# Kernel optimization log

Hardware: AMD Instinct MI355X
Metric: run time of the kernel (lower is better)

## Reference

```python
import jax, jax.numpy as jnp
import numpy as np

# --- MLA config (matches init_kwargs) ---
DIM = 2048
H = 16
KV_RANK = 512
Q_RANK = 1536
ROPE = 64          # qk_rope_head_dim (even)
NOPE = 128         # qk_nope_head_dim
VD = 128           # v_head_dim
THETA = 500000.0
EPS = 1e-6
B, T = 1, 2048
QK_HEAD = NOPE + ROPE  # logits use nope + rope dims


def _rmsnorm(x, w):
    # x float32; RMS over last dim, no mean subtraction
    rms = jax.lax.rsqrt(jnp.mean(x * x, axis=-1, keepdims=True) + EPS)
    return (x * rms) * w


def _rope_tables(t):
    inv_freq = 1.0 / (THETA ** (jnp.arange(0, ROPE, 2, dtype=jnp.float32) / ROPE))  # (ROPE/2,)
    pos = jnp.arange(t, dtype=jnp.float32)
    angles = jnp.outer(pos, inv_freq)  # (T, ROPE/2)
    return jnp.cos(angles), jnp.sin(angles)


def _apply_rope(x, cos, sin):
    # x: (B, T, Hx, D) with adjacent-pair rotation; cos/sin: (T, D/2)
    b, t, h, d = x.shape
    xp = x.reshape(b, t, h, d // 2, 2)
    even, odd = xp[..., 0], xp[..., 1]
    c = cos.reshape(1, t, 1, d // 2)
    s = sin.reshape(1, t, 1, d // 2)
    out = jnp.stack((even * c - odd * s, odd * c + even * s), axis=-1)
    return out.reshape(b, t, h, d)


def setup_inputs() -> dict:
    key = jax.random.key(0)
    ks = jax.random.split(key, 7)
    s = 0.02
    x = jax.random.normal(ks[0], (B, T, DIM), dtype=jnp.float32)
    w_q_down = jax.random.normal(ks[1], (Q_RANK, DIM), dtype=jnp.float32) * s
    q_norm_w = jnp.ones((Q_RANK,), dtype=jnp.float32)
    w_q_up = jax.random.normal(ks[2], (H * (NOPE + ROPE), Q_RANK), dtype=jnp.float32) * s
    w_kv_down = jax.random.normal(ks[3], (KV_RANK + ROPE, DIM), dtype=jnp.float32) * s
    kv_norm_w = jnp.ones((KV_RANK,), dtype=jnp.float32)
    w_kv_up = jax.random.normal(ks[4], (H * (NOPE + VD), KV_RANK), dtype=jnp.float32) * s
    w_o = jax.random.normal(ks[5], (DIM, H * VD), dtype=jnp.float32) * s
    return {"x": x, "w_q_down": w_q_down, "q_norm_w": q_norm_w, "w_q_up": w_q_up,
            "w_kv_down": w_kv_down, "kv_norm_w": kv_norm_w, "w_kv_up": w_kv_up, "w_o": w_o}


def reference(x, w_q_down, q_norm_w, w_q_up, w_kv_down, kv_norm_w, w_kv_up, w_o):
    b, t, _ = x.shape
    # Query path: down-proj -> RMSNorm -> up-proj, split nope/rope
    c_q = _rmsnorm(x @ w_q_down.T, q_norm_w)                       # (B,T,Q_RANK)
    q = (c_q @ w_q_up.T).reshape(b, t, H, NOPE + ROPE)
    q_nope, q_rope = q[..., :NOPE], q[..., NOPE:]
    # KV path: down-proj -> split latent c_kv and shared rope key
    kv = x @ w_kv_down.T                                           # (B,T,KV_RANK+ROPE)
    c_kv = kv[..., :KV_RANK]
    k_rope_raw = kv[..., KV_RANK:].reshape(b, t, 1, ROPE)
    # RoPE (adjacent-pair), start_pos=0
    cos, sin = _rope_tables(t)
    q_rope = _apply_rope(q_rope, cos, sin)
    k_rope = _apply_rope(k_rope_raw, cos, sin)                     # (B,T,1,ROPE) shared head
    # Reconstruct k_nope and v from normalized latent
    kv_up = (_rmsnorm(c_kv, kv_norm_w) @ w_kv_up.T).reshape(b, t, H, NOPE + VD)
    k_nope, v = kv_up[..., :NOPE], kv_up[..., NOPE:]
    # Assemble full q/k (rope key broadcast across heads)
    q_full = jnp.concatenate((q_nope, q_rope), axis=-1)            # (B,T,H,QK_HEAD)
    k_full = jnp.concatenate((k_nope, jnp.broadcast_to(k_rope, (b, t, H, ROPE))), axis=-1)
    # Causal attention
    scale = 1.0 / np.sqrt(QK_HEAD)
    scores = jnp.einsum('bqhd,bkhd->bhqk', q_full, k_full) * scale  # (B,H,T,T)
    causal = jnp.tril(jnp.ones((t, t), dtype=bool))
    scores = jnp.where(causal[None, None], scores, -jnp.inf)
    attn = jax.nn.softmax(scores, axis=-1)
    out = jnp.einsum('bhqk,bkhd->bqhd', attn, v).reshape(b, t, H * VD)
    return out @ w_o.T                                             # (B,T,DIM)
```

## Files before the change

kernel.cpp:

```cpp
#include <hip/hip_runtime.h>
#include <hip/hip_bf16.h>

typedef short short8 __attribute__((ext_vector_type(8)));
typedef float f32x4 __attribute__((ext_vector_type(4)));

#define DIM 2048
#define NH 16
#define KV_RANK 512
#define Q_RANK 1536
#define ROPE_D 64
#define NOPE 128
#define VD 128
#define TT 2048
#define QKH 192
#define QD (NH * QKH)
#define KVUP_D (NH * (NOPE + VD))
#define WDN 2176

__device__ inline unsigned short f2bf(float f) {
  __hip_bfloat16 h = __float2bfloat16(f);
  union { __hip_bfloat16 h; unsigned short u; } cv; cv.h = h; return cv.u;
}
__device__ inline float bf2f(unsigned short u) {
  union { unsigned int i; float f; } cv; cv.i = ((unsigned int)u) << 16; return cv.f;
}
__device__ inline void gload_lds16(const void* g, void* l) {
  __builtin_amdgcn_global_load_lds(
      (const __attribute__((address_space(1))) void*)g,
      (__attribute__((address_space(3))) void*)l, 16, 0, 0);
}

__global__ __launch_bounds__(256) void convert_all(
    const float* __restrict__ x, const float* __restrict__ wqd,
    const float* __restrict__ wkvd, const float* __restrict__ wqu,
    const float* __restrict__ wkvu, const float* __restrict__ wo,
    unsigned short* __restrict__ xb, unsigned short* __restrict__ wdb,
    unsigned short* __restrict__ wqub, unsigned short* __restrict__ wkvub,
    unsigned short* __restrict__ wob) {
  int i = blockIdx.x * 256 + threadIdx.x;
  const int n0 = TT * DIM / 4;
  const int n1 = WDN * 2048 / 4;
  const int n2 = QD * Q_RANK / 4;
  const int n3 = KVUP_D * KV_RANK / 4;
  const int n4 = DIM * DIM / 4;
  float4 v;
  unsigned short* dst;
  if (i < n0) { v = reinterpret_cast<const float4*>(x)[i]; dst = xb; }
  else if ((i -= n0) < n1) {
    int row = i >> 9, c4 = i & 511;
    if (row < 1536)      v = reinterpret_cast<const float4*>(wqd)[row * 512 + c4];
    else if (row < 2112) v = reinterpret_cast<const float4*>(wkvd)[(row - 1536) * 512 + c4];
    else                 v = make_float4(0.f, 0.f, 0.f, 0.f);
    dst = wdb;
  }
  else if ((i -= n1) < n2) { v = reinterpret_cast<const float4*>(wqu)[i]; dst = wqub; }
  else if ((i -= n2) < n3) { v = reinterpret_cast<const float4*>(wkvu)[i]; dst = wkvub; }
  else if ((i -= n3) < n4) { v = reinterpret_cast<const float4*>(wo)[i]; dst = wob; }
  else return;
  ushort4 o;
  o.x = f2bf(v.x); o.y = f2bf(v.y); o.z = f2bf(v.z); o.w = f2bf(v.w);
  reinterpret_cast<ushort4*>(dst)[i] = o;
}

__device__ __forceinline__ void gemm_core(const unsigned short* __restrict__ A,
                                          const unsigned short* __restrict__ W,
                                          unsigned short* As, unsigned short* Bs,
                                          int K, int lda, int ldb,
                                          int bm, int bn, int tid,
                                          f32x4 (&acc)[4][4]) {
  const int lane = tid & 63, wave = tid >> 6;
  const int wm = (wave >> 1) * 64, wn = (wave & 1) * 64;
  const int fr = lane & 15, fg = lane >> 4;
  const int sr = lane >> 3, scb = (lane & 7) ^ sr;
  const int r0 = wave * 32;

  const unsigned short* Ag = A + (size_t)(bm + r0 + sr) * lda + scb * 8;
  const unsigned short* Wg = W + (size_t)(bn + r0 + sr) * ldb + scb * 8;
  const int nt = K >> 6;

#pragma unroll
  for (int i = 0; i < 4; ++i) {
    gload_lds16(Ag + (size_t)(i * 8) * lda, As + r0 * 64 + i * 512);
    gload_lds16(Wg + (size_t)(i * 8) * ldb, Bs + r0 * 64 + i * 512);
  }
  int cur = 0;
  for (int t = 0; t < nt; ++t) {
    if (t + 1 < nt) {
      const int nb = cur ^ 1;
      const int ko = (t + 1) * 64;
#pragma unroll
      for (int i = 0; i < 4; ++i) {
        gload_lds16(Ag + ko + (size_t)(i * 8) * lda, As + nb * 8192 + r0 * 64 + i * 512);
        gload_lds16(Wg + ko + (size_t)(i * 8) * ldb, Bs + nb * 8192 + r0 * 64 + i * 512);
      }
      asm volatile("s_waitcnt vmcnt(8)" ::: "memory");
    } else {
      asm volatile("s_waitcnt vmcnt(0)" ::: "memory");
    }
    __builtin_amdgcn_s_barrier();
    asm volatile("" ::: "memory");
    const unsigned short* Ac = As + cur * 8192;
    const unsigned short* Bc = Bs + cur * 8192;
    __builtin_amdgcn_s_setprio(1);
#pragma unroll
    for (int kk = 0; kk < 2; ++kk) {
      short8 a[4], b[4];
#pragma unroll
      for (int i = 0; i < 4; ++i) {
        int ra = wm + i * 16 + fr;
        a[i] = *reinterpret_cast<const short8*>(&Ac[ra * 64 + (((kk * 4 + fg) ^ (ra & 7)) * 8)]);
        int rb = wn + i * 16 + fr;
        b[i] = *reinterpret_cast<const short8*>(&Bc[rb * 64 + (((kk * 4 + fg) ^ (rb & 7)) * 8)]);
      }
#pragma unroll
      for (int i = 0; i < 4; ++i)
#pragma unroll
        for (int j = 0; j < 4; ++j)
          acc[i][j] = __builtin_amdgcn_mfma_f32_16x16x32_bf16(a[i], b[j], acc[i][j], 0, 0, 0);
    }
    __builtin_amdgcn_s_setprio(0);
    asm volatile("" ::: "memory");
    __builtin_amdgcn_s_barrier();
    cur ^= 1;
  }
}

__global__ __launch_bounds__(256) void gemm_fast(const unsigned short* __restrict__ A,
                                                 const unsigned short* __restrict__ W,
                                                 float* __restrict__ Cf,
                                                 unsigned short* __restrict__ Cb,
                                                 int K, int lda, int ldb, int ldc) {
  __shared__ __align__(16) unsigned short As[2 * 128 * 64];
  __shared__ __align__(16) unsigned short Bs[2 * 128 * 64];
  const int tid = threadIdx.x;
  const int bm = blockIdx.y * 128, bn = blockIdx.x * 128;
  const int lane = tid & 63, wave = tid >> 6;
  const int wm = (wave >> 1) * 64, wn = (wave & 1) * 64;
  const int fr = lane & 15, fg = lane >> 4;

  f32x4 acc[4][4] = {};
  gemm_core(A, W, As, Bs, K, lda, ldb, bm, bn, tid, acc);

  if (Cb) {
#pragma unroll
    for (int i = 0; i < 4; ++i) {
      int row0 = bm + wm + i * 16 + fg * 4;
#pragma unroll
      for (int j = 0; j < 4; ++j) {
        int col = bn + wn + j * 16 + fr;
#pragma unroll
        for (int r = 0; r < 4; ++r)
          Cb[(size_t)(row0 + r) * ldc + col] = f2bf(acc[i][j][r]);
      }
    }
  } else {
#pragma unroll
    for (int i = 0; i < 4; ++i) {
      int row0 = bm + wm + i * 16 + fg * 4;
#pragma unroll
      for (int j = 0; j < 4; ++j) {
        int col = bn + wn + j * 16 + fr;
#pragma unroll
        for (int r = 0; r < 4; ++r)
          Cf[(size_t)(row0 + r) * ldc + col] = acc[i][j][r];
      }
    }
  }
}

__global__ __launch_bounds__(256) void gemm_dual(
    const unsigned short* __restrict__ A1, const unsigned short* __restrict__ W1,
    unsigned short* __restrict__ C1,
    const unsigned short* __restrict__ A2, const unsigned short* __restrict__ W2,
    unsigned short* __restrict__ C2, unsigned short* __restrict__ vt) {
  __shared__ __align__(16) unsigned short As[2 * 128 * 64];
  __shared__ __align__(16) unsigned short Bs[2 * 128 * 64];
  const int tid = threadIdx.x;
  const int bx = blockIdx.x;
  const unsigned short *A, *W;
  unsigned short* C;
  int K, lda, ldc, bm, bn;
  bool vwrite = false;
  if (bx < 384) {
    A = A1; W = W1; C = C1; K = Q_RANK; lda = Q_RANK; ldc = QD;
    bn = (bx % 24) * 128; bm = (bx / 24) * 128;
  } else {
    int b2 = bx - 384;
    A = A2; W = W2; C = C2; K = KV_RANK; lda = KV_RANK; ldc = KVUP_D;
    bn = (b2 & 31) * 128; bm = (b2 >> 5) * 128;
    vwrite = (bn & 128) != 0;
  }
  const int lane = tid & 63, wave = tid >> 6;
  const int wm = (wave >> 1) * 64, wn = (wave & 1) * 64;
  const int fr = lane & 15, fg = lane >> 4;

  f32x4 acc[4][4] = {};
  gemm_core(A, W, As, Bs, K, lda, lda, bm, bn, tid, acc);

#pragma unroll
  for (int i = 0; i < 4; ++i) {
    int row0 = bm + wm + i * 16 + fg * 4;
#pragma unroll
    for (int j = 0; j < 4; ++j) {
      int col = bn + wn + j * 16 + fr;
#pragma unroll
      for (int r = 0; r < 4; ++r)
        C[(size_t)(row0 + r) * ldc + col] = f2bf(acc[i][j][r]);
    }
  }
  if (vwrite) {
    const int hh = bn >> 8;
#pragma unroll
    for (int i = 0; i < 4; ++i) {
      int t0r = bm + wm + i * 16 + fg * 4;
#pragma unroll
      for (int j = 0; j < 4; ++j) {
        int d = wn + j * 16 + fr;
        ushort4 w4;
        w4.x = f2bf(acc[i][j][0]); w4.y = f2bf(acc[i][j][1]);
        w4.z = f2bf(acc[i][j][2]); w4.w = f2bf(acc[i][j][3]);
        *reinterpret_cast<ushort4*>(vt + (size_t)(hh * VD + d) * TT + t0r) = w4;
      }
    }
  }
}

__global__ __launch_bounds__(256) void rmsnorm_bf16(const unsigned short* __restrict__ in,
                                                    int instride, int inoff,
                                                    const float* __restrict__ w,
                                                    unsigned short* __restrict__ out,
                                                    int outstride, int cols) {
  const int row = blockIdx.x, tid = threadIdx.x;
  const unsigned short* x = in + (size_t)row * instride + inoff;
  const int nch = cols >> 3;
  float ss = 0.f;
  for (int cb = tid; cb < nch; cb += 256) {
    short8 v = *reinterpret_cast<const short8*>(x + cb * 8);
#pragma unroll
    for (int e = 0; e < 8; ++e) { float f = bf2f((unsigned short)v[e]); ss += f * f; }
  }
  __shared__ float red[256];
  red[tid] = ss; __syncthreads();
  for (int off = 128; off > 0; off >>= 1) {
    if (tid < off) red[tid] += red[tid + off];
    __syncthreads();
  }
  float r = rsqrtf(red[0] / (float)cols + 1e-6f);
  for (int cb = tid; cb < nch; cb += 256) {
    short8 v = *reinterpret_cast<const short8*>(x + cb * 8);
    ushort4 o0, o1;
    o0.x = f2bf(bf2f((unsigned short)v[0]) * r * w[cb * 8 + 0]);
    o0.y = f2bf(bf2f((unsigned short)v[1]) * r * w[cb * 8 + 1]);
    o0.z = f2bf(bf2f((unsigned short)v[2]) * r * w[cb * 8 + 2]);
    o0.w = f2bf(bf2f((unsigned short)v[3]) * r * w[cb * 8 + 3]);
    o1.x = f2bf(bf2f((unsigned short)v[4]) * r * w[cb * 8 + 4]);
    o1.y = f2bf(bf2f((unsigned short)v[5]) * r * w[cb * 8 + 5]);
    o1.z = f2bf(bf2f((unsigned short)v[6]) * r * w[cb * 8 + 6]);
    o1.w = f2bf(bf2f((unsigned short)v[7]) * r * w[cb * 8 + 7]);
    *reinterpret_cast<ushort4*>(out + (size_t)row * outstride + cb * 8) = o0;
    *reinterpret_cast<ushort4*>(out + (size_t)row * outstride + cb * 8 + 4) = o1;
  }
}

__global__ __launch_bounds__(256) void rope_kernel(unsigned short* __restrict__ qb,
                                                   const unsigned short* __restrict__ cqkv,
                                                   unsigned short* __restrict__ kr) {
  const int t = blockIdx.x, tid = threadIdx.x;
  unsigned short* qrow = qb + (size_t)t * QD;
  for (int p = tid; p < NH * 32 + 32; p += 256) {
    int j = (p < NH * 32) ? (p & 31) : (p - NH * 32);
    float inv = powf(500000.0f, -(float)(2 * j) * (1.0f / 64.0f));
    float ang = (float)t * inv;
    float sv, cv;
    sincosf(ang, &sv, &cv);
    if (p < NH * 32) {
      int h = p >> 5;
      unsigned short* b = qrow + h * QKH + NOPE + 2 * j;
      float e = bf2f(b[0]), o = bf2f(b[1]);
      b[0] = f2bf(e * cv - o * sv);
      b[1] = f2bf(o * cv + e * sv);
    } else {
      const unsigned short* b = cqkv + (size_t)t * WDN + 2048 + 2 * j;
      float e = bf2f(b[0]), o = bf2f(b[1]);
      kr[(size_t)t * ROPE_D + 2 * j]     = f2bf(e * cv - o * sv);
      kr[(size_t)t * ROPE_D + 2 * j + 1] = f2bf(o * cv + e * sv);
    }
  }
}

__global__ __launch_bounds__(256) void attn_part(
    const unsigned short* __restrict__ qb,
    const unsigned short* __restrict__ kvupb,
    const unsigned short* __restrict__ kropeb,
    const unsigned short* __restrict__ vtb,
    unsigned short* __restrict__ Opart,
    float* __restrict__ ml)
{
  const int b = (int)gridDim.x - 1 - (int)blockIdx.x;
  const int h = b / 80;
  const int w = b - h * 80;
  int qi, c;
  if (w < 8)       { qi = w;                  c = 0; }
  else if (w < 24) { qi = 8 + ((w - 8) >> 1);  c = (w - 8) & 1; }
  else if (w < 48) { qi = 16 + (w - 24) / 3;   c = (w - 24) % 3; }
  else             { qi = 24 + ((w - 48) >> 2); c = (w - 48) & 3; }
  const int t0 = qi * 64;
  const int ktlo = c * 8;
  const int kthi = min(ktlo + 8, qi + 1);
  const int tid = threadIdx.x;
  const int lane = tid & 63, wave = tid >> 6;
  const int fr = lane & 15, fg = lane >> 4;

  __shared__ __align__(16) unsigned short Ks[64 * 192];
  __shared__ __align__(16) unsigned short Vs[128 * 64];
  __shared__ __align__(16) unsigned short Ps[4][16 * 64];

  short8 qf[6];
  {
    const unsigned short* qrow = qb + (size_t)(t0 + wave * 16 + fr) * QD + h * QKH;
#pragma unroll
    for (int kc = 0; kc < 6; ++kc)
      qf[kc] = *reinterpret_cast<const short8*>(qrow + kc * 32 + fg * 8);
  }

  f32x4 o[8] = {};
  float m[4] = {-1e30f, -1e30f, -1e30f, -1e30f};
  float l[4] = {0.f, 0.f, 0.f, 0.f};
  const float scale = 0.0721687836487032f;

  for (int kt = ktlo; kt < kthi; ++kt) {
    const int kt0 = kt * 64;
#pragma unroll
    for (int i = 0; i < 6; ++i) {
      int u = tid + i * 256;
      int row = u / 24, cb = u - (u / 24) * 24;
      int cbs = cb ^ (row & 7);
      const unsigned short* src = (cb < 16)
        ? kvupb + (size_t)(kt0 + row) * KVUP_D + h * 256 + cbs * 8
        : kropeb + (size_t)(kt0 + row) * ROPE_D + (cbs - 16) * 8;
      gload_lds16(src, Ks + u * 8);
    }
#pragma unroll
    for (int i = 0; i < 4; ++i) {
      int u = tid + i * 256;
      int d = u >> 3, cb = u & 7;
      int cbs = cb ^ (d & 7);
      gload_lds16(vtb + (size_t)(h * VD + d) * TT + kt0 + cbs * 8, Vs + u * 8);
    }
    __syncthreads();

    f32x4 s[4] = {};
    __builtin_amdgcn_s_setprio(1);
#pragma unroll
    for (int kc = 0; kc < 6; ++kc) {
#pragma unroll
      for (int jj = 0; jj < 4; ++jj) {
        int rb = jj * 16 + fr;
        short8 bb = *reinterpret_cast<const short8*>(
            &Ks[rb * 192 + (((kc * 4 + fg) ^ (rb & 7)) * 8)]);
        s[jj] = __builtin_amdgcn_mfma_f32_16x16x32_bf16(qf[kc], bb, s[jj], 0, 0, 0);
      }
    }
    __builtin_amdgcn_s_setprio(0);

    const bool diag = (kt == qi);
#pragma unroll
    for (int r = 0; r < 4; ++r) {
      float sv[4];
#pragma unroll
      for (int jj = 0; jj < 4; ++jj) {
        float xx = s[jj][r] * scale;
        if (diag && (jj * 16 + fr) > (wave * 16 + fg * 4 + r)) xx = -1e30f;
        sv[jj] = xx;
      }
      float mx = fmaxf(fmaxf(sv[0], sv[1]), fmaxf(sv[2], sv[3]));
#pragma unroll
      for (int off = 1; off < 16; off <<= 1)
        mx = fmaxf(mx, __shfl_xor(mx, off));
      if (mx > m[r]) {
        float corr = __expf(m[r] - mx);
        m[r] = mx;
        l[r] *= corr;
#pragma unroll
        for (int dj = 0; dj < 8; ++dj) o[dj][r] *= corr;
      }
      float ssum = 0.f;
      float p[4];
#pragma unroll
      for (int jj = 0; jj < 4; ++jj) {
        p[jj] = __expf(sv[jj] - m[r]);
        ssum += p[jj];
      }
#pragma unroll
      for (int off = 1; off < 16; off <<= 1)
        ssum += __shfl_xor(ssum, off);
      l[r] += ssum;
      int prow = fg * 4 + r;
#pragma unroll
      for (int jj = 0; jj < 4; ++jj)
        Ps[wave][prow * 64 + ((jj * 16 + fr) ^ ((prow & 7) << 3))] = f2bf(p[jj]);
    }

    __builtin_amdgcn_s_setprio(1);
#pragma unroll
    for (int kc = 0; kc < 2; ++kc) {
      short8 p = *reinterpret_cast<const short8*>(
          &Ps[wave][fr * 64 + (((kc * 4 + fg) ^ (fr & 7)) * 8)]);
#pragma unroll
      for (int dj = 0; dj < 8; ++dj) {
        int rv = dj * 16 + fr;
        short8 bb = *reinterpret_cast<const short8*>(
            &Vs[rv * 64 + (((kc * 4 + fg) ^ (rv & 7)) * 8)]);
        o[dj] = __builtin_amdgcn_mfma_f32_16x16x32_bf16(p, bb, o[dj], 0, 0, 0);
      }
    }
    __builtin_amdgcn_s_setprio(0);
    __syncthreads();
  }

  const int slot = (h * 32 + qi) * 4 + c;
#pragma unroll
  for (int r = 0; r < 4; ++r) {
    int row = wave * 16 + fg * 4 + r;
    unsigned short* orow = Opart + ((size_t)slot * 64 + row) * 128;
#pragma unroll
    for (int dj = 0; dj < 8; ++dj)
      orow[dj * 16 + fr] = f2bf(o[dj][r]);
    if (fr == 0) {
      ml[((size_t)slot * 64 + row) * 2]     = m[r];
      ml[((size_t)slot * 64 + row) * 2 + 1] = l[r];
    }
  }
}

__global__ __launch_bounds__(256) void attn_combine(
    const unsigned short* __restrict__ Opart, const float* __restrict__ ml,
    unsigned short* __restrict__ out) {
  const int bid = blockIdx.x;
  const int h = bid >> 5, qi = bid & 31;
  const int nch = (qi >> 3) + 1;
  const int tid = threadIdx.x;
  const int row = tid >> 2, dg = tid & 3;
  const int base = bid * 4;
  float mm[4], ll[4];
  float M = -1e30f;
#pragma unroll
  for (int cc = 0; cc < 4; ++cc) {
    if (cc < nch) {
      mm[cc] = ml[((size_t)(base + cc) * 64 + row) * 2];
      ll[cc] = ml[((size_t)(base + cc) * 64 + row) * 2 + 1];
      M = fmaxf(M, mm[cc]);
    } else { mm[cc] = -1e30f; ll[cc] = 0.f; }
  }
  float L = 0.f;
#pragma unroll
  for (int cc = 0; cc < 4; ++cc) {
    mm[cc] = __expf(mm[cc] - M);
    L += ll[cc] * mm[cc];
  }
  float acc[32] = {};
#pragma unroll
  for (int cc = 0; cc < 4; ++cc) {
    if (cc < nch) {
      const unsigned short* op = Opart + ((size_t)(base + cc) * 64 + row) * 128 + dg * 32;
      float sc = mm[cc];
#pragma unroll
      for (int e8 = 0; e8 < 4; ++e8) {
        short8 v = *reinterpret_cast<const short8*>(op + e8 * 8);
#pragma unroll
        for (int e = 0; e < 8; ++e) acc[e8 * 8 + e] += bf2f((unsigned short)v[e]) * sc;
      }
    }
  }
  float linv = 1.0f / L;
  unsigned short* dst = out + (size_t)(qi * 64 + row) * DIM + h * VD + dg * 32;
#pragma unroll
  for (int e4 = 0; e4 < 8; ++e4) {
    ushort4 w4;
    w4.x = f2bf(acc[e4 * 4 + 0] * linv);
    w4.y = f2bf(acc[e4 * 4 + 1] * linv);
    w4.z = f2bf(acc[e4 * 4 + 2] * linv);
    w4.w = f2bf(acc[e4 * 4 + 3] * linv);
    *reinterpret_cast<ushort4*>(dst + e4 * 4) = w4;
  }
}

extern "C" void kernel_launch(void* const* d_in, const int* in_sizes, int n_in,
                              void* d_out, int out_size, void* d_ws, size_t ws_size,
                              hipStream_t stream) {
  const float* x        = (const float*)d_in[0];
  const float* w_q_down = (const float*)d_in[1];
  const float* q_norm_w = (const float*)d_in[2];
  const float* w_q_up   = (const float*)d_in[3];
  const float* w_kv_down= (const float*)d_in[4];
  const float* kv_norm_w= (const float*)d_in[5];
  const float* w_kv_up  = (const float*)d_in[6];
  const float* w_o      = (const float*)d_in[7];
  float* outp = (float*)d_out;

  char* ws = (char*)d_ws;
  size_t off = 0;
  auto alloc = [&](size_t bytes) {
    void* p = ws + off;
    off += (bytes + 255) & ~(size_t)255;
    return p;
  };
  unsigned short* x_bf     = (unsigned short*)alloc((size_t)TT * DIM * 2);
  unsigned short* wdown_bf = (unsigned short*)alloc((size_t)WDN * DIM * 2);
  unsigned short* wqu_bf   = (unsigned short*)alloc((size_t)QD * Q_RANK * 2);
  unsigned short* wkvu_bf  = (unsigned short*)alloc((size_t)KVUP_D * KV_RANK * 2);
  unsigned short* wo_bf    = (unsigned short*)alloc((size_t)DIM * DIM * 2);
  unsigned short* cqkv_bf  = (unsigned short*)alloc((size_t)TT * WDN * 2);
  unsigned short* cq_bf    = (unsigned short*)alloc((size_t)TT * Q_RANK * 2);
  unsigned short* ckv_bf   = (unsigned short*)alloc((size_t)TT * KV_RANK * 2);
  unsigned short* qb_bf    = (unsigned short*)alloc((size_t)TT * QD * 2);
  unsigned short* kvup_bf  = (unsigned short*)alloc((size_t)TT * KVUP_D * 2);
  unsigned short* krope_bf = (unsigned short*)alloc((size_t)TT * ROPE_D * 2);
  unsigned short* vtb      = (unsigned short*)alloc((size_t)NH * VD * TT * 2);
  unsigned short* Opart    = (unsigned short*)alloc((size_t)2048 * 64 * 128 * 2);
  float*          mlbuf    = (float*)alloc((size_t)2048 * 64 * 2 * 4);
  unsigned short* attn_bf  = x_bf;

  {
    int total = TT * DIM / 4 + WDN * 2048 / 4 + QD * Q_RANK / 4 +
                KVUP_D * KV_RANK / 4 + DIM * DIM / 4;
    convert_all<<<dim3((total + 255) / 256), dim3(256), 0, stream>>>(
        x, w_q_down, w_kv_down, w_q_up, w_kv_up, w_o,
        x_bf, wdown_bf, wqu_bf, wkvu_bf, wo_bf);
  }

  dim3 blk(256);
  gemm_fast<<<dim3(WDN / 128, TT / 128), blk, 0, stream>>>(
      x_bf, wdown_bf, nullptr, cqkv_bf, DIM, DIM, DIM, WDN);
  rmsnorm_bf16<<<dim3(TT), blk, 0, stream>>>(cqkv_bf, WDN, 0, q_norm_w, cq_bf, Q_RANK, Q_RANK);
  rmsnorm_bf16<<<dim3(TT), blk, 0, stream>>>(cqkv_bf, WDN, Q_RANK, kv_norm_w, ckv_bf, KV_RANK, KV_RANK);
  gemm_dual<<<dim3(896), blk, 0, stream>>>(cq_bf, wqu_bf, qb_bf,
                                           ckv_bf, wkvu_bf, kvup_bf, vtb);
  rope_kernel<<<dim3(TT), blk, 0, stream>>>(qb_bf, cqkv_bf, krope_bf);
  attn_part<<<dim3(1280), blk, 0, stream>>>(qb_bf, kvup_bf, krope_bf, vtb, Opart, mlbuf);
  attn_combine<<<dim3(512), blk, 0, stream>>>(Opart, mlbuf, attn_bf);
  gemm_fast<<<dim3(DIM / 128, TT / 128), blk, 0, stream>>>(
      attn_bf, wo_bf, outp, nullptr, DIM, DIM, DIM, DIM);
}
```

Measured before the change: 245.3 us.

## Restructure attention partial kernel with 128-row Q tiles and double-buffered KV

The attention partial kernel now processes 128 query rows per block, with each wave owning two 16-row slices. It iterates 32-key tiles through a double-buffered LDS stage so the next tile's global-to-LDS loads overlap the current tile's compute. It computes S transposed (K as the A operand) so the softmax row reduction needs only two cross-lane shuffles, and it skips the output rescale when no row's max changed. It also uses padded LDS rows instead of XOR swizzles and reorders blocks to schedule heavy causal tiles first, with the combine kernel and buffers adjusted to the new 128-row layout. The cost is fewer blocks (640) and more registers per thread, which may lower occupancy.

```diff
diff --git a/kernel.cpp b/kernel.cpp
--- a/kernel.cpp
+++ b/kernel.cpp
@@ -296,139 +296,184 @@
     unsigned short* __restrict__ Opart,
     float* __restrict__ ml)
 {
-  const int b = (int)gridDim.x - 1 - (int)blockIdx.x;
-  const int h = b / 80;
-  const int w = b - h * 80;
-  int qi, c;
-  if (w < 8)       { qi = w;                  c = 0; }
-  else if (w < 24) { qi = 8 + ((w - 8) >> 1);  c = (w - 8) & 1; }
-  else if (w < 48) { qi = 16 + (w - 24) / 3;   c = (w - 24) % 3; }
-  else             { qi = 24 + ((w - 48) >> 2); c = (w - 48) & 3; }
-  const int t0 = qi * 64;
-  const int ktlo = c * 8;
-  const int kthi = min(ktlo + 8, qi + 1);
+  const int b = blockIdx.x;
+  const int h = b & 15;
+  const int w = b >> 4;
+  int qt, c;
+  if (w < 16)      { qt = 15 - (w >> 2); c = w & 3; }
+  else if (w < 28) { int v = w - 16; qt = 11 - v / 3; c = v % 3; }
+  else if (w < 36) { int v = w - 28; qt = 7 - (v >> 1); c = v & 1; }
+  else             { qt = 3 - (w - 36); c = 0; }
+  const int t0 = qt * 128;
+  const int ktlo = c * 16;
+  const int kthi = min(ktlo + 16, 4 * qt + 4);
   const int tid = threadIdx.x;
-  const int lane = tid & 63, wave = tid >> 6;
+  const int lane = tid & 63, wv = tid >> 6;
   const int fr = lane & 15, fg = lane >> 4;
 
-  __shared__ __align__(16) unsigned short Ks[64 * 192];
-  __shared__ __align__(16) unsigned short Vs[128 * 64];
-  __shared__ __align__(16) unsigned short Ps[4][16 * 64];
-
-  short8 qf[6];
-  {
-    const unsigned short* qrow = qb + (size_t)(t0 + wave * 16 + fr) * QD + h * QKH;
-#pragma unroll
-    for (int kc = 0; kc < 6; ++kc)
-      qf[kc] = *reinterpret_cast<const short8*>(qrow + kc * 32 + fg * 8);
-  }
-
-  f32x4 o[8] = {};
-  float m[4] = {-1e30f, -1e30f, -1e30f, -1e30f};
-  float l[4] = {0.f, 0.f, 0.f, 0.f};
-  const float scale = 0.0721687836487032f;
-
-  for (int kt = ktlo; kt < kthi; ++kt) {
-    const int kt0 = kt * 64;
+  __shared__ __align__(16) unsigned short KV[2][1536 * 8];
+  __shared__ __align__(16) unsigned short Ps[4][2][16 * 36];
+
+  auto STAGE = [&](int bufi, int kt) {
 #pragma unroll
     for (int i = 0; i < 6; ++i) {
       int u = tid + i * 256;
-      int row = u / 24, cb = u - (u / 24) * 24;
-      int cbs = cb ^ (row & 7);
-      const unsigned short* src = (cb < 16)
-        ? kvupb + (size_t)(kt0 + row) * KVUP_D + h * 256 + cbs * 8
-        : kropeb + (size_t)(kt0 + row) * ROPE_D + (cbs - 16) * 8;
-      gload_lds16(src, Ks + u * 8);
-    }
-#pragma unroll
-    for (int i = 0; i < 4; ++i) {
-      int u = tid + i * 256;
-      int d = u >> 3, cb = u & 7;
-      int cbs = cb ^ (d & 7);
-      gload_lds16(vtb + (size_t)(h * VD + d) * TT + kt0 + cbs * 8, Vs + u * 8);
-    }
-    __syncthreads();
-
-    f32x4 s[4] = {};
+      const unsigned short* src;
+      if (u < 800) {
+        int row = u / 25, cb = u - row * 25;
+        if (cb >= 24) cb = 0;
+        src = (cb < 16)
+          ? kvupb + (size_t)(kt * 32 + row) * KVUP_D + h * 256 + cb * 8
+          : kropeb + (size_t)(kt * 32 + row) * ROPE_D + (cb - 16) * 8;
+      } else if (u < 1440) {
+        int v2 = u - 800;
+        int d = v2 / 5, cb = v2 - d * 5;
+        if (cb >= 4) cb = 0;
+        src = vtb + (size_t)(h * VD + d) * TT + kt * 32 + cb * 8;
+      } else {
+        src = kvupb;
+      }
+      gload_lds16(src, &KV[bufi][u * 8]);
+    }
+  };
+
+  STAGE(0, ktlo);
+
+  short8 qf[2][6];
+#pragma unroll
+  for (int s = 0; s < 2; ++s) {
+    const unsigned short* qrow = qb + (size_t)(t0 + wv * 32 + s * 16 + fr) * QD + h * QKH;
+#pragma unroll
+    for (int kc = 0; kc < 6; ++kc)
+      qf[s][kc] = *reinterpret_cast<const short8*>(qrow + kc * 32 + fg * 8);
+  }
+
+  f32x4 o[2][8] = {};
+  float m2[2] = {-1e30f, -1e30f};
+  float l2[2] = {0.f, 0.f};
+  const float scale = 0.0721687836487032f;
+
+  int buf = 0;
+  for (int kt = ktlo; kt < kthi; ++kt) {
+    if (kt + 1 < kthi) {
+      STAGE(buf ^ 1, kt + 1);
+      asm volatile("s_waitcnt vmcnt(6)" ::: "memory");
+    } else {
+      asm volatile("s_waitcnt vmcnt(0)" ::: "memory");
+    }
+    __builtin_amdgcn_s_barrier();
+    asm volatile("" ::: "memory");
+    const unsigned short* Kb = KV[buf];
+    const unsigned short* Vb = KV[buf] + 6400;
+
+    f32x4 sA[2][2] = {};
     __builtin_amdgcn_s_setprio(1);
 #pragma unroll
     for (int kc = 0; kc < 6; ++kc) {
 #pragma unroll
-      for (int jj = 0; jj < 4; ++jj) {
-        int rb = jj * 16 + fr;
-        short8 bb = *reinterpret_cast<const short8*>(
-            &Ks[rb * 192 + (((kc * 4 + fg) ^ (rb & 7)) * 8)]);
-        s[jj] = __builtin_amdgcn_mfma_f32_16x16x32_bf16(qf[kc], bb, s[jj], 0, 0, 0);
+      for (int jj = 0; jj < 2; ++jj) {
+        int row = jj * 16 + fr;
+        short8 kf = *reinterpret_cast<const short8*>(&Kb[row * 200 + (kc * 4 + fg) * 8]);
+        sA[0][jj] = __builtin_amdgcn_mfma_f32_16x16x32_bf16(kf, qf[0][kc], sA[0][jj], 0, 0, 0);
+        sA[1][jj] = __builtin_amdgcn_mfma_f32_16x16x32_bf16(kf, qf[1][kc], sA[1][jj], 0, 0, 0);
       }
     }
     __builtin_amdgcn_s_setprio(0);
 
-    const bool diag = (kt == qi);
+    const bool diag = (kt >= 4 * qt);
+#pragma unroll
+    for (int s = 0; s < 2; ++s) {
+      const int qg = t0 + wv * 32 + s * 16 + fr;
+      float mx = -1e30f;
+#pragma unroll
+      for (int jj = 0; jj < 2; ++jj)
+#pragma unroll
+        for (int r = 0; r < 4; ++r) {
+          float svv = sA[s][jj][r] * scale;
+          if (diag && (kt * 32 + jj * 16 + fg * 4 + r) > qg) svv = -1e30f;
+          sA[s][jj][r] = svv;
+          mx = fmaxf(mx, svv);
+        }
+      mx = fmaxf(mx, __shfl_xor(mx, 16));
+      mx = fmaxf(mx, __shfl_xor(mx, 32));
+      float mn = fmaxf(m2[s], mx);
+      float corr = __expf(m2[s] - mn);
+      m2[s] = mn;
+      float ssum = 0.f;
+      float p[8];
+#pragma unroll
+      for (int jj = 0; jj < 2; ++jj)
+#pragma unroll
+        for (int r = 0; r < 4; ++r) {
+          float pv = __expf(sA[s][jj][r] - mn);
+          p[jj * 4 + r] = pv;
+          ssum += pv;
+        }
+      ssum += __shfl_xor(ssum, 16);
+      ssum += __shfl_xor(ssum, 32);
+      l2[s] = l2[s] * corr + ssum;
+#pragma unroll
+      for (int jj = 0; jj < 2; ++jj) {
+        ushort4 pk;
+        pk.x = f2bf(p[jj * 4 + 0]);
+        pk.y = f2bf(p[jj * 4 + 1]);
+        pk.z = f2bf(p[jj * 4 + 2]);
+        pk.w = f2bf(p[jj * 4 + 3]);
+        *reinterpret_cast<ushort4*>(&Ps[wv][s][fr * 36 + jj * 16 + fg * 4]) = pk;
+      }
+      if (__any(corr != 1.0f)) {
+        float c0 = __shfl(corr, fg * 4 + 0);
+        float c1 = __shfl(corr, fg * 4 + 1);
+        float c2 = __shfl(corr, fg * 4 + 2);
+        float c3 = __shfl(corr, fg * 4 + 3);
+#pragma unroll
+        for (int dj = 0; dj < 8; ++dj) {
+          o[s][dj][0] *= c0; o[s][dj][1] *= c1;
+          o[s][dj][2] *= c2; o[s][dj][3] *= c3;
+        }
+      }
+    }
+
+    short8 pa[2];
+#pragma unroll
+    for (int s = 0; s < 2; ++s) {
+      const unsigned short* pp = &Ps[wv][s][fr * 36 + fg * 8];
+      ushort4 lo = *reinterpret_cast<const ushort4*>(pp);
+      ushort4 hi = *reinterpret_cast<const ushort4*>(pp + 4);
+      short8 t;
+      t[0] = (short)lo.x; t[1] = (short)lo.y; t[2] = (short)lo.z; t[3] = (short)lo.w;
+      t[4] = (short)hi.x; t[5] = (short)hi.y; t[6] = (short)hi.z; t[7] = (short)hi.w;
+      pa[s] = t;
+    }
+    __builtin_amdgcn_s_setprio(1);
+#pragma unroll
+    for (int dj = 0; dj < 8; ++dj) {
+      int rv = dj * 16 + fr;
+      short8 bv = *reinterpret_cast<const short8*>(&Vb[rv * 40 + fg * 8]);
+      o[0][dj] = __builtin_amdgcn_mfma_f32_16x16x32_bf16(pa[0], bv, o[0][dj], 0, 0, 0);
+      o[1][dj] = __builtin_amdgcn_mfma_f32_16x16x32_bf16(pa[1], bv, o[1][dj], 0, 0, 0);
+    }
+    __builtin_amdgcn_s_setprio(0);
+    asm volatile("" ::: "memory");
+    __builtin_amdgcn_s_barrier();
+    buf ^= 1;
+  }
+
+  const int slot = (h * 16 + qt) * 4 + c;
+#pragma unroll
+  for (int s = 0; s < 2; ++s) {
 #pragma unroll
     for (int r = 0; r < 4; ++r) {
-      float sv[4];
-#pragma unroll
-      for (int jj = 0; jj < 4; ++jj) {
-        float xx = s[jj][r] * scale;
-        if (diag && (jj * 16 + fr) > (wave * 16 + fg * 4 + r)) xx = -1e30f;
-        sv[jj] = xx;
-      }
-      float mx = fmaxf(fmaxf(sv[0], sv[1]), fmaxf(sv[2], sv[3]));
-#pragma unroll
-      for (int off = 1; off < 16; off <<= 1)
-        mx = fmaxf(mx, __shfl_xor(mx, off));
-      if (mx > m[r]) {
-        float corr = __expf(m[r] - mx);
-        m[r] = mx;
-        l[r] *= corr;
-#pragma unroll
-        for (int dj = 0; dj < 8; ++dj) o[dj][r] *= corr;
-      }
-      float ssum = 0.f;
-      float p[4];
-#pragma unroll
-      for (int jj = 0; jj < 4; ++jj) {
-        p[jj] = __expf(sv[jj] - m[r]);
-        ssum += p[jj];
-      }
-#pragma unroll
-      for (int off = 1; off < 16; off <<= 1)
-        ssum += __shfl_xor(ssum, off);
-      l[r] += ssum;
-      int prow = fg * 4 + r;
-#pragma unroll
-      for (int jj = 0; jj < 4; ++jj)
-        Ps[wave][prow * 64 + ((jj * 16 + fr) ^ ((prow & 7) << 3))] = f2bf(p[jj]);
-    }
-
-    __builtin_amdgcn_s_setprio(1);
-#pragma unroll
-    for (int kc = 0; kc < 2; ++kc) {
-      short8 p = *reinterpret_cast<const short8*>(
-          &Ps[wave][fr * 64 + (((kc * 4 + fg) ^ (fr & 7)) * 8)]);
-#pragma unroll
-      for (int dj = 0; dj < 8; ++dj) {
-        int rv = dj * 16 + fr;
-        short8 bb = *reinterpret_cast<const short8*>(
-            &Vs[rv * 64 + (((kc * 4 + fg) ^ (rv & 7)) * 8)]);
-        o[dj] = __builtin_amdgcn_mfma_f32_16x16x32_bf16(p, bb, o[dj], 0, 0, 0);
-      }
-    }
-    __builtin_amdgcn_s_setprio(0);
-    __syncthreads();
-  }
-
-  const int slot = (h * 32 + qi) * 4 + c;
-#pragma unroll
-  for (int r = 0; r < 4; ++r) {
-    int row = wave * 16 + fg * 4 + r;
-    unsigned short* orow = Opart + ((size_t)slot * 64 + row) * 128;
-#pragma unroll
-    for (int dj = 0; dj < 8; ++dj)
-      orow[dj * 16 + fr] = f2bf(o[dj][r]);
-    if (fr == 0) {
-      ml[((size_t)slot * 64 + row) * 2]     = m[r];
-      ml[((size_t)slot * 64 + row) * 2 + 1] = l[r];
+      int row = wv * 32 + s * 16 + fg * 4 + r;
+      unsigned short* orow = Opart + ((size_t)slot * 128 + row) * 128;
+#pragma unroll
+      for (int dj = 0; dj < 8; ++dj)
+        orow[dj * 16 + fr] = f2bf(o[s][dj][r]);
+    }
+    if (fg == 0) {
+      int row = wv * 32 + s * 16 + fr;
+      ml[((size_t)slot * 128 + row) * 2]     = m2[s];
+      ml[((size_t)slot * 128 + row) * 2 + 1] = l2[s];
     }
   }
 }
@@ -437,18 +482,20 @@
     const unsigned short* __restrict__ Opart, const float* __restrict__ ml,
     unsigned short* __restrict__ out) {
   const int bid = blockIdx.x;
-  const int h = bid >> 5, qi = bid & 31;
-  const int nch = (qi >> 3) + 1;
+  const int h = bid >> 5;
+  const int qt = (bid >> 1) & 15;
+  const int rh = bid & 1;
+  const int nch = qt / 4 + 1;
   const int tid = threadIdx.x;
-  const int row = tid >> 2, dg = tid & 3;
-  const int base = bid * 4;
+  const int row = rh * 64 + (tid >> 2), dg = tid & 3;
+  const int base = (h * 16 + qt) * 4;
   float mm[4], ll[4];
   float M = -1e30f;
 #pragma unroll
   for (int cc = 0; cc < 4; ++cc) {
     if (cc < nch) {
-      mm[cc] = ml[((size_t)(base + cc) * 64 + row) * 2];
-      ll[cc] = ml[((size_t)(base + cc) * 64 + row) * 2 + 1];
+      mm[cc] = ml[((size_t)(base + cc) * 128 + row) * 2];
+      ll[cc] = ml[((size_t)(base + cc) * 128 + row) * 2 + 1];
       M = fmaxf(M, mm[cc]);
     } else { mm[cc] = -1e30f; ll[cc] = 0.f; }
   }
@@ -462,7 +509,7 @@
 #pragma unroll
   for (int cc = 0; cc < 4; ++cc) {
     if (cc < nch) {
-      const unsigned short* op = Opart + ((size_t)(base + cc) * 64 + row) * 128 + dg * 32;
+      const unsigned short* op = Opart + ((size_t)(base + cc) * 128 + row) * 128 + dg * 32;
       float sc = mm[cc];
 #pragma unroll
       for (int e8 = 0; e8 < 4; ++e8) {
@@ -473,7 +520,7 @@
     }
   }
   float linv = 1.0f / L;
-  unsigned short* dst = out + (size_t)(qi * 64 + row) * DIM + h * VD + dg * 32;
+  unsigned short* dst = out + (size_t)(qt * 128 + row) * DIM + h * VD + dg * 32;
 #pragma unroll
   for (int e4 = 0; e4 < 8; ++e4) {
     ushort4 w4;
@@ -517,8 +564,8 @@
   unsigned short* kvup_bf  = (unsigned short*)alloc((size_t)TT * KVUP_D * 2);
   unsigned short* krope_bf = (unsigned short*)alloc((size_t)TT * ROPE_D * 2);
   unsigned short* vtb      = (unsigned short*)alloc((size_t)NH * VD * TT * 2);
-  unsigned short* Opart    = (unsigned short*)alloc((size_t)2048 * 64 * 128 * 2);
-  float*          mlbuf    = (float*)alloc((size_t)2048 * 64 * 2 * 4);
+  unsigned short* Opart    = (unsigned short*)alloc((size_t)1024 * 128 * 128 * 2);
+  float*          mlbuf    = (float*)alloc((size_t)1024 * 128 * 2 * 4);
   unsigned short* attn_bf  = x_bf;
 
   {
@@ -537,7 +584,7 @@
   gemm_dual<<<dim3(896), blk, 0, stream>>>(cq_bf, wqu_bf, qb_bf,
                                            ckv_bf, wkvu_bf, kvup_bf, vtb);
   rope_kernel<<<dim3(TT), blk, 0, stream>>>(qb_bf, cqkv_bf, krope_bf);
-  attn_part<<<dim3(1280), blk, 0, stream>>>(qb_bf, kvup_bf, krope_bf, vtb, Opart, mlbuf);
+  attn_part<<<dim3(640), blk, 0, stream>>>(qb_bf, kvup_bf, krope_bf, vtb, Opart, mlbuf);
   attn_combine<<<dim3(512), blk, 0, stream>>>(Opart, mlbuf, attn_bf);
   gemm_fast<<<dim3(DIM / 128, TT / 128), blk, 0, stream>>>(
       attn_bf, wo_bf, outp, nullptr, DIM, DIM, DIM, DIM);
```

Measured after the change: 272.9 us. 1.11x slower.
